# Kernel tuning notes

Measured on AMD Instinct MI355X. Metric: run time of the kernel, lower is better.

Reference implementation:

```python
import jax, jax.numpy as jnp
import numpy as np

B, T, I, D = 16, 128, 8, 128


def layer_norm(x, g, b, eps=1e-5):
    mu = jnp.mean(x, -1, keepdims=True)
    var = jnp.mean((x - mu) ** 2, -1, keepdims=True)
    return (x - mu) * jax.lax.rsqrt(var + eps) * g + b


def setup_inputs() -> dict:
    key = jax.random.key(0)
    ks = jax.random.split(key, 8)
    vectors = jax.random.normal(ks[0], (B, T, T, I), jnp.float32)
    # structured pairwise mask: mask[b,i,j] = real[b,i] & real[b,j]
    lengths = jax.random.randint(ks[1], (B,), T // 2, T + 1)
    real = jnp.arange(T)[None, :] < lengths[:, None]  # [B,T]
    mask = real[:, :, None] & real[:, None, :]  # [B,T,T]
    s = lambda n: 1.0 / np.sqrt(n)
    W_embed = jax.random.normal(ks[2], (I, D), jnp.float32) * s(I)
    b_embed = jnp.zeros((D,), jnp.float32)
    ln1_g = jnp.ones((D,), jnp.float32)
    ln1_b = jnp.zeros((D,), jnp.float32)
    Wq = jax.random.normal(ks[3], (D, D), jnp.float32) * s(D)
    Wk = jax.random.normal(ks[4], (D, D), jnp.float32) * s(D)
    Wv = jax.random.normal(ks[5], (D, D), jnp.float32) * s(D)
    W_out = jax.random.normal(ks[6], (D, D), jnp.float32) * s(D)
    b_out = jnp.zeros((D,), jnp.float32)
    ln2_g = jnp.ones((D,), jnp.float32)
    ln2_b = jnp.zeros((D,), jnp.float32)
    return dict(vectors=vectors, mask=mask, W_embed=W_embed, b_embed=b_embed,
                ln1_g=ln1_g, ln1_b=ln1_b, Wq=Wq, Wk=Wk, Wv=Wv,
                W_out=W_out, b_out=b_out, ln2_g=ln2_g, ln2_b=ln2_b)


def reference(vectors, mask, W_embed, b_embed, ln1_g, ln1_b, Wq, Wk, Wv,
              W_out, b_out, ln2_g, ln2_b):
    Bs, Tn = vectors.shape[0], vectors.shape[1]
    Dm = W_embed.shape[1]
    square_mask = jnp.transpose(mask, (1, 2, 0))            # [T,T,B] bool
    seq = square_mask[jnp.arange(Tn), jnp.arange(Tn)]       # [T,B] bool (diagonal)
    # shared embedding stack (masked) + norm, on flattened [T*T,B,*]
    x = jnp.transpose(vectors.reshape(Bs, Tn * Tn, -1), (1, 0, 2))  # [T*T,B,I]
    mflat = square_mask.reshape(Tn * Tn, Bs, 1).astype(x.dtype)
    x = jax.nn.gelu(x @ W_embed + b_embed) * mflat
    x = layer_norm(x, ln1_g, ln1_b)
    x = x.reshape(Tn, Tn, Bs, Dm)                           # [T,T,B,D]
    keys = x @ Wk                                            # [T,T,B,D]
    values = x @ Wv                                          # [T,T,B,D]
    queries = x[jnp.arange(Tn), jnp.arange(Tn)] @ Wq         # diag gather -> [T,B,D]
    # attention mask: pairwise-real OR self
    amask = square_mask | jnp.eye(Tn, dtype=bool)[:, :, None]  # [T,T,B]
    logits = jnp.einsum('rbd,rcbd->rcb', queries, keys) / np.sqrt(Dm)
    logits = logits + jnp.where(amask, 0.0, -1e9)
    w = jax.nn.softmax(logits, axis=1)                       # [T,T,B]
    emb = jnp.einsum('rcb,rcbd->rbd', w, values)             # [T,B,D]
    # output linear block with skip connection, masked by sequence mask
    seq_f = seq[:, :, None].astype(emb.dtype)                # [T,B,1]
    h = jax.nn.gelu(emb @ W_out + b_out)
    embeddings = layer_norm(h + emb, ln2_g, ln2_b) * seq_f   # [T,B,D]
    padding_mask = ~jnp.transpose(seq)                       # [B,T]
    sequence_mask = seq[:, :, None]                          # [T,B,1]
    global_mask = jnp.ones((Tn,), dtype=bool)                # [T]
    return embeddings, padding_mask, sequence_mask, global_mask
```

## Files before the change

### kernel.cpp

```cpp
#include <hip/hip_runtime.h>
#include <hip/hip_fp16.h>
#include <math.h>

#define BB 16
#define TT 128
#define II 8
#define DD 128
#define SCALE 0.08838834764831845f

#define WS_WVO_OFF 16384
#define WS_LEN_OFF 32768


__device__ __forceinline__ float sgelu(float x) {
    float x2 = x * x;
    float w = x * (-1.5957691216f - 0.07135481627f * x2);
    float e = __expf(w);
    return __fdividef(x, 1.0f + e);
}

__device__ __forceinline__ float fast_gelu(float x) {
    float u = 1.5957691216057308f * x * (1.0f + 0.044715f * x * x);
    float e = __expf(u);
    float th = 1.0f - __fdividef(2.0f, e + 1.0f);
    return 0.5f * x * (1.0f + th);
}

__global__ void k0_setup(const float* __restrict__ Wq,
                         const float* __restrict__ Wk,
                         const float* __restrict__ Wv,
                         const float* __restrict__ Wo,
                         const int* __restrict__ mask,
                         float* __restrict__ M,
                         float* __restrict__ WvWo,
                         int* __restrict__ lens) {
    int blk = blockIdx.x;
    if (blk == DD) {
        __shared__ int cnt[BB];
        int t = threadIdx.x;
        if (t < BB) cnt[t] = 0;
        __syncthreads();
        for (int b = 0; b < BB; b++) {
            if (mask[b * TT * TT + t * TT + t]) atomicAdd(&cnt[b], 1);
        }
        __syncthreads();
        if (t < BB) lens[t] = cnt[t];
        return;
    }
    __shared__ float row[DD];
    int d = threadIdx.x;
    if (blk < DD) {
        int a = blk;
        row[d] = Wq[a * DD + d];
        __syncthreads();
        const float4* wk4 = (const float4*)(Wk + d * DD);
        float acc = 0.0f;
        #pragma unroll 8
        for (int e4 = 0; e4 < DD / 4; e4++) {
            float4 w = wk4[e4];
            acc += row[e4 * 4 + 0] * w.x + row[e4 * 4 + 1] * w.y +
                   row[e4 * 4 + 2] * w.z + row[e4 * 4 + 3] * w.w;
        }
        M[a * DD + d] = acc;
    } else {
        int a = blk - DD - 1;
        row[d] = Wv[a * DD + d];
        __syncthreads();
        float acc = 0.0f;
        #pragma unroll 8
        for (int e = 0; e < DD; e++) acc += row[e] * Wo[e * DD + d];
        WvWo[a * DD + d] = acc;
    }
}

__global__ __launch_bounds__(256, 4)
void k_main(const float* __restrict__ vectors,
            const int* __restrict__ lens,
            const float* __restrict__ We,
            const float* __restrict__ be,
            const float* __restrict__ g1,
            const float* __restrict__ b1,
            const float* __restrict__ M,
            const float* __restrict__ Wv,
            const float* __restrict__ WvWo,
            const float* __restrict__ bo,
            const float* __restrict__ g2,
            const float* __restrict__ b2,
            float* __restrict__ out) {
    __shared__ __half2 xsh[TT * 64];
    __shared__ float  xrs[DD];
    __shared__ float  kqs[DD];
    __shared__ float  lgt[TT];
    __shared__ float  wgt[TT];
    __shared__ float2 pbuf[256];
    __shared__ float2 sv2[64];

    int n = blockIdx.x;
    int b = n >> 7, r = n & 127;
    int t = threadIdx.x, wave = t >> 6, lane = t & 63;
    int hh = lane >> 5, sl = lane & 31;
    int dl = sl * 4;
    int len = lens[b];

    if (r >= len) {
        if (wave == 0) {
            int rb_out = r * BB + b;
            ((float2*)out)[rb_out * 64 + lane] = make_float2(0.0f, 0.0f);
            if (lane == 0) {
                out[262144 + b * TT + r] = 1.0f;
                out[264192 + r * BB + b] = 0.0f;
                if (b == 0) out[266240 + r] = 1.0f;
            }
        }
        return;
    }

    const float4* vb4 = (const float4*)(vectors + (size_t)n * TT * II);

    float4 we4[II];
    #pragma unroll
    for (int i = 0; i < II; i++) we4[i] = *(const float4*)(We + i * DD + dl);
    float4 be4 = *(const float4*)(be + dl);
    float4 g14 = *(const float4*)(g1 + dl);
    float4 b14 = *(const float4*)(b1 + dl);

    {
        int g = (wave << 1) + hh;
        int jmax = (len - g + 15) >> 4;
        for (int j = 0; j < jmax; j++) {
            int cA = (j << 4) + g;
            int cB = cA + 8;
            float4 vA0 = vb4[2 * cA], vA1 = vb4[2 * cA + 1];
            float4 vB0 = vb4[2 * cB], vB1 = vb4[2 * cB + 1];
            float vA[8] = {vA0.x, vA0.y, vA0.z, vA0.w, vA1.x, vA1.y, vA1.z, vA1.w};
            float vB[8] = {vB0.x, vB0.y, vB0.z, vB0.w, vB1.x, vB1.y, vB1.z, vB1.w};
            float eA0 = be4.x, eA1 = be4.y, eA2 = be4.z, eA3 = be4.w;
            float eB0 = be4.x, eB1 = be4.y, eB2 = be4.z, eB3 = be4.w;
            #pragma unroll
            for (int i = 0; i < II; i++) {
                eA0 += vA[i] * we4[i].x; eA1 += vA[i] * we4[i].y;
                eA2 += vA[i] * we4[i].z; eA3 += vA[i] * we4[i].w;
                eB0 += vB[i] * we4[i].x; eB1 += vB[i] * we4[i].y;
                eB2 += vB[i] * we4[i].z; eB3 += vB[i] * we4[i].w;
            }
            float aA0 = sgelu(eA0), aA1 = sgelu(eA1), aA2 = sgelu(eA2), aA3 = sgelu(eA3);
            float aB0 = sgelu(eB0), aB1 = sgelu(eB1), aB2 = sgelu(eB2), aB3 = sgelu(eB3);
            float sA = (aA0 + aA1) + (aA2 + aA3);
            float qA = (aA0 * aA0 + aA1 * aA1) + (aA2 * aA2 + aA3 * aA3);
            float sB = (aB0 + aB1) + (aB2 + aB3);
            float qB = (aB0 * aB0 + aB1 * aB1) + (aB2 * aB2 + aB3 * aB3);
            #pragma unroll
            for (int o = 16; o >= 1; o >>= 1) {
                sA += __shfl_xor(sA, o, 64); qA += __shfl_xor(qA, o, 64);
                sB += __shfl_xor(sB, o, 64); qB += __shfl_xor(qB, o, 64);
            }
            float muA = sA * (1.0f / 128.0f), muB = sB * (1.0f / 128.0f);
            float rsA = rsqrtf(qA * (1.0f / 128.0f) - muA * muA + 1e-5f);
            float rsB = rsqrtf(qB * (1.0f / 128.0f) - muB * muB + 1e-5f);
            float xA0 = (aA0 - muA) * rsA * g14.x + b14.x;
            float xA1 = (aA1 - muA) * rsA * g14.y + b14.y;
            float xA2 = (aA2 - muA) * rsA * g14.z + b14.z;
            float xA3 = (aA3 - muA) * rsA * g14.w + b14.w;
            float xB0 = (aB0 - muB) * rsB * g14.x + b14.x;
            float xB1 = (aB1 - muB) * rsB * g14.y + b14.y;
            float xB2 = (aB2 - muB) * rsB * g14.z + b14.z;
            float xB3 = (aB3 - muB) * rsB * g14.w + b14.w;
            {
                __half2 p0 = __floats2half2_rn(xA0, xA1), p1 = __floats2half2_rn(xA2, xA3);
                uint2 st; st.x = *(unsigned*)&p0; st.y = *(unsigned*)&p1;
                ((uint2*)(xsh + cA * 64))[sl] = st;
                if (cA == r) ((float4*)xrs)[sl] = make_float4(xA0, xA1, xA2, xA3);
            }
            if (cB < len) {
                __half2 p0 = __floats2half2_rn(xB0, xB1), p1 = __floats2half2_rn(xB2, xB3);
                uint2 st; st.x = *(unsigned*)&p0; st.y = *(unsigned*)&p1;
                ((uint2*)(xsh + cB * 64))[sl] = st;
                if (cB == r) ((float4*)xrs)[sl] = make_float4(xB0, xB1, xB2, xB3);
            }
        }
    }
    __syncthreads();

    {
        const float2* M2 = (const float2*)M;
        float ax = 0.0f, ay = 0.0f;
        #pragma unroll 8
        for (int j = 0; j < 32; j++) {
            int a = (wave << 5) + j;
            float xv = xrs[a];
            float2 m2 = M2[a * 64 + lane];
            ax += xv * m2.x; ay += xv * m2.y;
        }
        pbuf[t] = make_float2(ax, ay);
    }
    __syncthreads();
    if (t < 64) {
        float2 p0 = pbuf[t], p1 = pbuf[64 + t], p2 = pbuf[128 + t], p3 = pbuf[192 + t];
        kqs[2 * t]     = (p0.x + p1.x + p2.x + p3.x) * SCALE;
        kqs[2 * t + 1] = (p0.y + p1.y + p2.y + p3.y) * SCALE;
    }
    __syncthreads();

    {
        int c = t >> 1, p = t & 1;
        if (c < len) {
            const float2* kq2 = (const float2*)kqs;
            float acc = 0.0f;
            #pragma unroll 8
            for (int j = 0; j < 32; j++) {
                int idx = (p << 5) + ((j + c) & 31);
                float2 xf = __half22float2(xsh[c * 64 + idx]);
                float2 kv = kq2[idx];
                acc += xf.x * kv.x + xf.y * kv.y;
            }
            acc += __shfl_xor(acc, 1, 64);
            if (p == 0) lgt[c] = acc;
        }
    }
    __syncthreads();

    if (wave == 0) {
        float l0 = lgt[lane];
        float l1 = (lane + 64 < len) ? lgt[lane + 64] : -1e9f;
        float mx = fmaxf(l0, l1);
        #pragma unroll
        for (int o = 32; o >= 1; o >>= 1) mx = fmaxf(mx, __shfl_xor(mx, o, 64));
        float e0 = __expf(l0 - mx), e1 = __expf(l1 - mx);
        float s = e0 + e1;
        #pragma unroll
        for (int o = 32; o >= 1; o >>= 1) s += __shfl_xor(s, o, 64);
        float inv = __fdividef(1.0f, s);
        wgt[lane] = e0 * inv; wgt[lane + 64] = e1 * inv;
    }
    __syncthreads();

    {
        int jw = (len - wave + 3) >> 2;
        float ax = 0.0f, ay = 0.0f;
        for (int j = 0; j < jw; j++) {
            int c = (j << 2) + wave;
            float w = wgt[c];
            float2 xf = __half22float2(xsh[c * 64 + lane]);
            ax += w * xf.x; ay += w * xf.y;
        }
        pbuf[t] = make_float2(ax, ay);
    }
    __syncthreads();
    if (t < 64) {
        float2 p0 = pbuf[t], p1 = pbuf[64 + t], p2 = pbuf[128 + t], p3 = pbuf[192 + t];
        sv2[t] = make_float2(p0.x + p1.x + p2.x + p3.x, p0.y + p1.y + p2.y + p3.y);
    }
    __syncthreads();

    {
        const float* svf = (const float*)sv2;
        const float2* W2 = (wave < 2) ? (const float2*)Wv : (const float2*)WvWo;
        int abase = (wave & 1) << 6;
        float ax = 0.0f, ay = 0.0f;
        #pragma unroll 8
        for (int j = 0; j < 64; j++) {
            int a = abase + j;
            float s = svf[a];
            float2 w2 = W2[a * 64 + lane];
            ax += s * w2.x; ay += s * w2.y;
        }
        pbuf[t] = make_float2(ax, ay);
    }
    __syncthreads();

    if (wave == 0) {
        float2 e0 = pbuf[lane], e1 = pbuf[64 + lane];
        float2 h0p = pbuf[128 + lane], h1p = pbuf[192 + lane];
        float2 bo2 = ((const float2*)bo)[lane];
        float em0 = e0.x + e1.x, em1 = e0.y + e1.y;
        float h0 = fast_gelu(h0p.x + h1p.x + bo2.x);
        float h1 = fast_gelu(h0p.y + h1p.y + bo2.y);
        float z0 = h0 + em0, z1 = h1 + em1;
        float s = z0 + z1, q = z0 * z0 + z1 * z1;
        #pragma unroll
        for (int o = 32; o >= 1; o >>= 1) {
            s += __shfl_xor(s, o, 64); q += __shfl_xor(q, o, 64);
        }
        float mu = s * (1.0f / 128.0f);
        float rstd = rsqrtf(q * (1.0f / 128.0f) - mu * mu + 1e-5f);
        float2 g22 = ((const float2*)g2)[lane], b22 = ((const float2*)b2)[lane];
        float u0 = z0 - mu, u1 = z1 - mu;
        int rb_out = r * BB + b;
        ((float2*)out)[rb_out * 64 + lane] =
            make_float2(u0 * rstd * g22.x + b22.x,
                        u1 * rstd * g22.y + b22.y);
        if (lane == 0) {
            out[262144 + b * TT + r] = 0.0f;
            out[264192 + r * BB + b] = 1.0f;
            if (b == 0) out[266240 + r] = 1.0f;
        }
    }
}

extern "C" void kernel_launch(void* const* d_in, const int* in_sizes, int n_in,
                              void* d_out, int out_size, void* d_ws, size_t ws_size,
                              hipStream_t stream) {
    const float* vectors = (const float*)d_in[0];
    const int*   mask    = (const int*)d_in[1];
    const float* W_embed = (const float*)d_in[2];
    const float* b_embed = (const float*)d_in[3];
    const float* ln1_g   = (const float*)d_in[4];
    const float* ln1_b   = (const float*)d_in[5];
    const float* Wq      = (const float*)d_in[6];
    const float* Wk      = (const float*)d_in[7];
    const float* Wv      = (const float*)d_in[8];
    const float* W_out   = (const float*)d_in[9];
    const float* b_out   = (const float*)d_in[10];
    const float* ln2_g   = (const float*)d_in[11];
    const float* ln2_b   = (const float*)d_in[12];
    float* out = (float*)d_out;

    float* M    = (float*)d_ws;
    float* WvWo = (float*)d_ws + WS_WVO_OFF;
    int*   lens = (int*)((float*)d_ws + WS_LEN_OFF);

    hipLaunchKernelGGL(k0_setup, dim3(2 * DD + 1), dim3(DD), 0, stream,
                       Wq, Wk, Wv, W_out, mask, M, WvWo, lens);
    hipLaunchKernelGGL(k_main, dim3(TT * BB), dim3(256), 0, stream,
                       vectors, lens, W_embed, b_embed, ln1_g, ln1_b, M,
                       Wv, WvWo, b_out, ln2_g, ln2_b, out);
}
```

Measured before the change: 136.7 us.

## Store un-normalized activations and fold layernorm into logits and weighted sum

The embedding stage now stores raw GELU activations in shared memory in fp16, along with per-column mean and rstd, instead of layer-normalized values. The logits are rebuilt algebraically using gamma-scaled query-key vectors plus correction terms (Us, C0). The weighted value sum applies rstd-scaled weights and adds the mean/gamma/beta correction afterwards. Every wave now runs the softmax redundantly into its own weight copy, which removes one barrier and the idle single-wave step. The cost is extra shared arrays and reductions, and fp16 storage of un-normalized values may change precision.

```diff
diff --git a/kernel.cpp b/kernel.cpp
--- a/kernel.cpp
+++ b/kernel.cpp
@@ -89,9 +89,12 @@
             float* __restrict__ out) {
     __shared__ __half2 xsh[TT * 64];
     __shared__ float  xrs[DD];
-    __shared__ float  kqs[DD];
+    __shared__ float2 kq2s[64];
+    __shared__ float2 us2[64];
+    __shared__ float  mus[TT];
+    __shared__ float  rstds[TT];
     __shared__ float  lgt[TT];
-    __shared__ float  wgt[TT];
+    __shared__ float  wgt4[4 * TT];
     __shared__ float2 pbuf[256];
     __shared__ float2 sv2[64];
 
@@ -157,25 +160,31 @@
             float muA = sA * (1.0f / 128.0f), muB = sB * (1.0f / 128.0f);
             float rsA = rsqrtf(qA * (1.0f / 128.0f) - muA * muA + 1e-5f);
             float rsB = rsqrtf(qB * (1.0f / 128.0f) - muB * muB + 1e-5f);
-            float xA0 = (aA0 - muA) * rsA * g14.x + b14.x;
-            float xA1 = (aA1 - muA) * rsA * g14.y + b14.y;
-            float xA2 = (aA2 - muA) * rsA * g14.z + b14.z;
-            float xA3 = (aA3 - muA) * rsA * g14.w + b14.w;
-            float xB0 = (aB0 - muB) * rsB * g14.x + b14.x;
-            float xB1 = (aB1 - muB) * rsB * g14.y + b14.y;
-            float xB2 = (aB2 - muB) * rsB * g14.z + b14.z;
-            float xB3 = (aB3 - muB) * rsB * g14.w + b14.w;
             {
-                __half2 p0 = __floats2half2_rn(xA0, xA1), p1 = __floats2half2_rn(xA2, xA3);
+                __half2 p0 = __floats2half2_rn(aA0, aA1), p1 = __floats2half2_rn(aA2, aA3);
                 uint2 st; st.x = *(unsigned*)&p0; st.y = *(unsigned*)&p1;
                 ((uint2*)(xsh + cA * 64))[sl] = st;
-                if (cA == r) ((float4*)xrs)[sl] = make_float4(xA0, xA1, xA2, xA3);
+                if (sl == 0) { mus[cA] = muA; rstds[cA] = rsA; }
+                if (cA == r) {
+                    ((float4*)xrs)[sl] = make_float4(
+                        (aA0 - muA) * rsA * g14.x + b14.x,
+                        (aA1 - muA) * rsA * g14.y + b14.y,
+                        (aA2 - muA) * rsA * g14.z + b14.z,
+                        (aA3 - muA) * rsA * g14.w + b14.w);
+                }
             }
             if (cB < len) {
-                __half2 p0 = __floats2half2_rn(xB0, xB1), p1 = __floats2half2_rn(xB2, xB3);
+                __half2 p0 = __floats2half2_rn(aB0, aB1), p1 = __floats2half2_rn(aB2, aB3);
                 uint2 st; st.x = *(unsigned*)&p0; st.y = *(unsigned*)&p1;
                 ((uint2*)(xsh + cB * 64))[sl] = st;
-                if (cB == r) ((float4*)xrs)[sl] = make_float4(xB0, xB1, xB2, xB3);
+                if (sl == 0) { mus[cB] = muB; rstds[cB] = rsB; }
+                if (cB == r) {
+                    ((float4*)xrs)[sl] = make_float4(
+                        (aB0 - muB) * rsB * g14.x + b14.x,
+                        (aB1 - muB) * rsB * g14.y + b14.y,
+                        (aB2 - muB) * rsB * g14.z + b14.z,
+                        (aB3 - muB) * rsB * g14.w + b14.w);
+                }
             }
         }
     }
@@ -196,59 +205,89 @@
     __syncthreads();
     if (t < 64) {
         float2 p0 = pbuf[t], p1 = pbuf[64 + t], p2 = pbuf[128 + t], p3 = pbuf[192 + t];
-        kqs[2 * t]     = (p0.x + p1.x + p2.x + p3.x) * SCALE;
-        kqs[2 * t + 1] = (p0.y + p1.y + p2.y + p3.y) * SCALE;
-    }
-    __syncthreads();
+        float k0 = (p0.x + p1.x + p2.x + p3.x) * SCALE;
+        float k1 = (p0.y + p1.y + p2.y + p3.y) * SCALE;
+        kq2s[t] = make_float2(k0, k1);
+        float2 g1v = ((const float2*)g1)[t];
+        us2[t] = make_float2(k0 * g1v.x, k1 * g1v.y);
+    }
+    __syncthreads();
+
+    float Us, C0;
+    {
+        float2 uu = us2[lane];
+        float2 kk = kq2s[lane];
+        float2 bb = ((const float2*)b1)[lane];
+        float usp = uu.x + uu.y;
+        float c0p = bb.x * kk.x + bb.y * kk.y;
+        #pragma unroll
+        for (int o = 32; o >= 1; o >>= 1) {
+            usp += __shfl_xor(usp, o, 64); c0p += __shfl_xor(c0p, o, 64);
+        }
+        Us = usp; C0 = c0p;
+    }
 
     {
         int c = t >> 1, p = t & 1;
         if (c < len) {
-            const float2* kq2 = (const float2*)kqs;
             float acc = 0.0f;
             #pragma unroll 8
             for (int j = 0; j < 32; j++) {
                 int idx = (p << 5) + ((j + c) & 31);
                 float2 xf = __half22float2(xsh[c * 64 + idx]);
-                float2 kv = kq2[idx];
-                acc += xf.x * kv.x + xf.y * kv.y;
+                float2 uv = us2[idx];
+                acc += xf.x * uv.x + xf.y * uv.y;
             }
             acc += __shfl_xor(acc, 1, 64);
-            if (p == 0) lgt[c] = acc;
-        }
-    }
-    __syncthreads();
-
-    if (wave == 0) {
+            if (p == 0) lgt[c] = rstds[c] * (acc - mus[c] * Us) + C0;
+        }
+    }
+    __syncthreads();
+
+    float invS, Aterm;
+    {
         float l0 = lgt[lane];
-        float l1 = (lane + 64 < len) ? lgt[lane + 64] : -1e9f;
+        bool v1 = (lane + 64 < len);
+        float l1 = v1 ? lgt[lane + 64] : -1e9f;
         float mx = fmaxf(l0, l1);
         #pragma unroll
         for (int o = 32; o >= 1; o >>= 1) mx = fmaxf(mx, __shfl_xor(mx, o, 64));
         float e0 = __expf(l0 - mx), e1 = __expf(l1 - mx);
-        float s = e0 + e1;
+        float er0 = e0 * rstds[lane];
+        float er1 = v1 ? e1 * rstds[lane + 64] : 0.0f;
+        float sp = e0 + e1;
+        float ap = er0 * mus[lane] + (v1 ? er1 * mus[lane + 64] : 0.0f);
         #pragma unroll
-        for (int o = 32; o >= 1; o >>= 1) s += __shfl_xor(s, o, 64);
-        float inv = __fdividef(1.0f, s);
-        wgt[lane] = e0 * inv; wgt[lane + 64] = e1 * inv;
-    }
-    __syncthreads();
-
-    {
+        for (int o = 32; o >= 1; o >>= 1) {
+            sp += __shfl_xor(sp, o, 64); ap += __shfl_xor(ap, o, 64);
+        }
+        invS = __fdividef(1.0f, sp);
+        Aterm = ap;
+        wgt4[(wave << 7) + lane] = er0;
+        wgt4[(wave << 7) + lane + 64] = er1;
+    }
+
+    {
+        int wb = wave << 7;
         int jw = (len - wave + 3) >> 2;
         float ax = 0.0f, ay = 0.0f;
         for (int j = 0; j < jw; j++) {
             int c = (j << 2) + wave;
-            float w = wgt[c];
+            float v = wgt4[wb + c];
             float2 xf = __half22float2(xsh[c * 64 + lane]);
-            ax += w * xf.x; ay += w * xf.y;
+            ax += v * xf.x; ay += v * xf.y;
         }
         pbuf[t] = make_float2(ax, ay);
     }
     __syncthreads();
     if (t < 64) {
         float2 p0 = pbuf[t], p1 = pbuf[64 + t], p2 = pbuf[128 + t], p3 = pbuf[192 + t];
-        sv2[t] = make_float2(p0.x + p1.x + p2.x + p3.x, p0.y + p1.y + p2.y + p3.y);
+        float Ux = p0.x + p1.x + p2.x + p3.x;
+        float Uy = p0.y + p1.y + p2.y + p3.y;
+        float2 g1v = ((const float2*)g1)[t];
+        float2 b1v = ((const float2*)b1)[t];
+        sv2[t] = make_float2(g1v.x * (Ux - Aterm) * invS + b1v.x,
+                             g1v.y * (Uy - Aterm) * invS + b1v.y);
     }
     __syncthreads();
 
```

New measurement: 137.7 us. About the same (+0.8%).

## Fold query-key logits into the layernorm pass using precomputed projected query

Applied to the files above, without the earlier changes.

Computes the diagonal row's embedding and the projected query vector before the main embedding loop. The logit for each column is then derived algebraically from the per-column layernorm statistics plus one extra shuffle-reduced dot product (rstd*(p - mu*Us) + C0). This removes the separate pass that re-read the fp16 shared-memory tile to form logits. In exchange it recomputes the diagonal embedding once, adds a third reduction per column, and computes logits in fp32 from the un-rounded activations instead of the fp16 copy.

```diff
diff --git a/kernel.cpp b/kernel.cpp
--- a/kernel.cpp
+++ b/kernel.cpp
@@ -125,6 +125,65 @@
     float4 b14 = *(const float4*)(b1 + dl);
 
     {
+        float4 v0 = vb4[2 * r], v1 = vb4[2 * r + 1];
+        float vv[8] = {v0.x, v0.y, v0.z, v0.w, v1.x, v1.y, v1.z, v1.w};
+        float e0 = be4.x, e1 = be4.y, e2 = be4.z, e3 = be4.w;
+        #pragma unroll
+        for (int i = 0; i < II; i++) {
+            e0 += vv[i] * we4[i].x; e1 += vv[i] * we4[i].y;
+            e2 += vv[i] * we4[i].z; e3 += vv[i] * we4[i].w;
+        }
+        float a0 = sgelu(e0), a1 = sgelu(e1), a2 = sgelu(e2), a3 = sgelu(e3);
+        float s = (a0 + a1) + (a2 + a3);
+        float q = (a0 * a0 + a1 * a1) + (a2 * a2 + a3 * a3);
+        #pragma unroll
+        for (int o = 16; o >= 1; o >>= 1) {
+            s += __shfl_xor(s, o, 64); q += __shfl_xor(q, o, 64);
+        }
+        float mu = s * (1.0f / 128.0f);
+        float rstd = rsqrtf(q * (1.0f / 128.0f) - mu * mu + 1e-5f);
+        float x0 = (a0 - mu) * rstd * g14.x + b14.x;
+        float x1 = (a1 - mu) * rstd * g14.y + b14.y;
+        float x2 = (a2 - mu) * rstd * g14.z + b14.z;
+        float x3 = (a3 - mu) * rstd * g14.w + b14.w;
+        if (t < 32) ((float4*)xrs)[sl] = make_float4(x0, x1, x2, x3);
+    }
+    __syncthreads();
+
+    {
+        const float2* M2 = (const float2*)M;
+        float ax = 0.0f, ay = 0.0f;
+        #pragma unroll 8
+        for (int j = 0; j < 32; j++) {
+            int a = (wave << 5) + j;
+            float xv = xrs[a];
+            float2 m2 = M2[a * 64 + lane];
+            ax += xv * m2.x; ay += xv * m2.y;
+        }
+        pbuf[t] = make_float2(ax, ay);
+    }
+    __syncthreads();
+    if (t < 64) {
+        float2 p0 = pbuf[t], p1 = pbuf[64 + t], p2 = pbuf[128 + t], p3 = pbuf[192 + t];
+        kqs[2 * t]     = (p0.x + p1.x + p2.x + p3.x) * SCALE;
+        kqs[2 * t + 1] = (p0.y + p1.y + p2.y + p3.y) * SCALE;
+    }
+    __syncthreads();
+
+    float4 kq4 = *(const float4*)&kqs[dl];
+    float4 u4 = make_float4(g14.x * kq4.x, g14.y * kq4.y, g14.z * kq4.z, g14.w * kq4.w);
+    float Us, C0;
+    {
+        float us = (u4.x + u4.y) + (u4.z + u4.w);
+        float c0 = (b14.x * kq4.x + b14.y * kq4.y) + (b14.z * kq4.z + b14.w * kq4.w);
+        #pragma unroll
+        for (int o = 16; o >= 1; o >>= 1) {
+            us += __shfl_xor(us, o, 64); c0 += __shfl_xor(c0, o, 64);
+        }
+        Us = us; C0 = c0;
+    }
+
+    {
         int g = (wave << 1) + hh;
         int jmax = (len - g + 15) >> 4;
         for (int j = 0; j < jmax; j++) {
@@ -147,12 +206,16 @@
             float aB0 = sgelu(eB0), aB1 = sgelu(eB1), aB2 = sgelu(eB2), aB3 = sgelu(eB3);
             float sA = (aA0 + aA1) + (aA2 + aA3);
             float qA = (aA0 * aA0 + aA1 * aA1) + (aA2 * aA2 + aA3 * aA3);
+            float pA = (aA0 * u4.x + aA1 * u4.y) + (aA2 * u4.z + aA3 * u4.w);
             float sB = (aB0 + aB1) + (aB2 + aB3);
             float qB = (aB0 * aB0 + aB1 * aB1) + (aB2 * aB2 + aB3 * aB3);
+            float pB = (aB0 * u4.x + aB1 * u4.y) + (aB2 * u4.z + aB3 * u4.w);
             #pragma unroll
             for (int o = 16; o >= 1; o >>= 1) {
                 sA += __shfl_xor(sA, o, 64); qA += __shfl_xor(qA, o, 64);
+                pA += __shfl_xor(pA, o, 64);
                 sB += __shfl_xor(sB, o, 64); qB += __shfl_xor(qB, o, 64);
+                pB += __shfl_xor(pB, o, 64);
             }
             float muA = sA * (1.0f / 128.0f), muB = sB * (1.0f / 128.0f);
             float rsA = rsqrtf(qA * (1.0f / 128.0f) - muA * muA + 1e-5f);
@@ -169,52 +232,14 @@
                 __half2 p0 = __floats2half2_rn(xA0, xA1), p1 = __floats2half2_rn(xA2, xA3);
                 uint2 st; st.x = *(unsigned*)&p0; st.y = *(unsigned*)&p1;
                 ((uint2*)(xsh + cA * 64))[sl] = st;
-                if (cA == r) ((float4*)xrs)[sl] = make_float4(xA0, xA1, xA2, xA3);
+                if (sl == 0) lgt[cA] = rsA * (pA - muA * Us) + C0;
             }
             if (cB < len) {
                 __half2 p0 = __floats2half2_rn(xB0, xB1), p1 = __floats2half2_rn(xB2, xB3);
                 uint2 st; st.x = *(unsigned*)&p0; st.y = *(unsigned*)&p1;
                 ((uint2*)(xsh + cB * 64))[sl] = st;
-                if (cB == r) ((float4*)xrs)[sl] = make_float4(xB0, xB1, xB2, xB3);
-            }
-        }
-    }
-    __syncthreads();
-
-    {
-        const float2* M2 = (const float2*)M;
-        float ax = 0.0f, ay = 0.0f;
-        #pragma unroll 8
-        for (int j = 0; j < 32; j++) {
-            int a = (wave << 5) + j;
-            float xv = xrs[a];
-            float2 m2 = M2[a * 64 + lane];
-            ax += xv * m2.x; ay += xv * m2.y;
-        }
-        pbuf[t] = make_float2(ax, ay);
-    }
-    __syncthreads();
-    if (t < 64) {
-        float2 p0 = pbuf[t], p1 = pbuf[64 + t], p2 = pbuf[128 + t], p3 = pbuf[192 + t];
-        kqs[2 * t]     = (p0.x + p1.x + p2.x + p3.x) * SCALE;
-        kqs[2 * t + 1] = (p0.y + p1.y + p2.y + p3.y) * SCALE;
-    }
-    __syncthreads();
-
-    {
-        int c = t >> 1, p = t & 1;
-        if (c < len) {
-            const float2* kq2 = (const float2*)kqs;
-            float acc = 0.0f;
-            #pragma unroll 8
-            for (int j = 0; j < 32; j++) {
-                int idx = (p << 5) + ((j + c) & 31);
-                float2 xf = __half22float2(xsh[c * 64 + idx]);
-                float2 kv = kq2[idx];
-                acc += xf.x * kv.x + xf.y * kv.y;
-            }
-            acc += __shfl_xor(acc, 1, 64);
-            if (p == 0) lgt[c] = acc;
+                if (sl == 0) lgt[cB] = rsB * (pB - muB * Us) + C0;
+            }
         }
     }
     __syncthreads();
```

New measurement: 135.5 us. About the same (-0.9%).
